# Kernel tuning notes

Measured on AMD Instinct MI355X. Metric: run time of the kernel, lower is better.

The kernel has to match this reference:

```python
import jax, jax.numpy as jnp
import numpy as np

B, G, T = 4096, 100, 24


def _greedy_dispatch(demand, caps, prices, slack_price):
    """Exact LP solution of: min prices@alloc + slack_price*slack
    s.t. 0<=alloc<=caps, sum(alloc)+slack = demand (per b,t).
    demand: [B,T] (nonneg), caps: [B,G,T], prices: [G], slack_price: scalar.
    Returns alloc [B,G,T], slack [B,T].
    """
    prices_all = jnp.concatenate([prices, slack_price[None]])        # [G+1]
    # slack capacity = demand itself (slack alone can absorb everything)
    caps_all = jnp.concatenate([caps, demand[:, None, :]], axis=1)    # [B,G+1,T]
    order = jnp.argsort(prices_all)                                   # merit order
    caps_s = caps_all[:, order, :]
    before = jnp.cumsum(caps_s, axis=1) - caps_s                      # capacity ahead in merit order
    alloc_s = jnp.clip(demand[:, None, :] - before, 0.0, caps_s)
    inv = jnp.argsort(order)
    alloc = alloc_s[:, inv, :]
    return alloc[:, :-1, :], alloc[:, -1, :]


def setup_inputs() -> dict:
    key = jax.random.key(0)
    k1, k2, k3, k4 = jax.random.split(key, 4)
    R_up = jax.random.uniform(k1, (B, G, T), dtype=jnp.float32)
    R_dn = jax.random.uniform(k2, (B, G, T), dtype=jnp.float32)
    omega_true = jax.random.normal(k3, (B, T), dtype=jnp.float32) * 5.0
    b_G = 10.0 + 40.0 * jax.random.uniform(k4, (G,), dtype=jnp.float32)  # marginal costs $/MWh
    return {
        "R_up": R_up,
        "R_dn": R_dn,
        "omega_true": omega_true,
        "b_G": b_G,
        "voll": jnp.float32(1000.0),
        "vosp": jnp.float32(500.0),
        "rt_up_ratio": jnp.float32(1.5),
        "rt_dn_ratio": jnp.float32(1.2),
    }


def reference(R_up, R_dn, omega_true, b_G, voll, vosp, rt_up_ratio, rt_dn_ratio):
    c_up = rt_up_ratio * b_G                                          # [G]
    c_dn = rt_dn_ratio * b_G                                          # [G]
    dem_up = jnp.maximum(omega_true, 0.0)                             # [B,T]
    dem_dn = jnp.maximum(-omega_true, 0.0)
    du, LS = _greedy_dispatch(dem_up, R_up, c_up, voll)
    dd, SP = _greedy_dispatch(dem_dn, R_dn, c_dn, vosp)
    rt_obj = (jnp.einsum('g,bgt->b', c_up, du)
              + jnp.einsum('g,bgt->b', c_dn, dd)
              + voll * LS.sum(axis=1) + vosp * SP.sum(axis=1))        # [B]
    return du, dd, LS, SP, rt_obj
```

## Files before the change

### kernel.cpp

```cpp
#include <hip/hip_runtime.h>

#define G_ 100
#define T_ 24
#define GP1 101
#define TILE (G_ * T_)
#define VPB (TILE / 4)
#define BPB 4
#define WPB (BPB * 2)
#define BLOCK (64 * WPB)

typedef float vfloat4 __attribute__((ext_vector_type(4)));

template<int N>
__device__ __forceinline__ void scan_chunk(int k0,
    const float* __restrict__ capp,
    float* __restrict__ gcol,
    int ord_lo, int ord_hi, float pr_lo, float pr_hi,
    float dem, float& before, float& objp)
{
    int gg[N]; float pr[N], cap[N];
#pragma unroll
    for (int j = 0; j < N; ++j) {
        const int idx = k0 + j;
        if (idx < 64) {
            gg[j] = __builtin_amdgcn_readlane(ord_lo, idx);
            pr[j] = __int_as_float(__builtin_amdgcn_readlane(__float_as_int(pr_lo), idx));
        } else {
            gg[j] = __builtin_amdgcn_readlane(ord_hi, idx - 64);
            pr[j] = __int_as_float(__builtin_amdgcn_readlane(__float_as_int(pr_hi), idx - 64));
        }
    }
#pragma unroll
    for (int j = 0; j < N; ++j) cap[j] = capp[gg[j] * T_];
#pragma unroll
    for (int j = 0; j < N; ++j) {
        float a = fminf(fmaxf(dem - before, 0.f), cap[j]);
        before += cap[j];
        objp = fmaf(pr[j], a, objp);
        gcol[gg[j] * T_] = a;
    }
}

__global__ __launch_bounds__(BLOCK, 8) void dispatch_kernel(
    const float* __restrict__ R_up, const float* __restrict__ R_dn,
    const float* __restrict__ omega,
    const float* __restrict__ b_G, const float* __restrict__ voll,
    const float* __restrict__ vosp, const float* __restrict__ ru,
    const float* __restrict__ rd,
    float* __restrict__ out, int B)
{
    __shared__ float s_praw[2][GP1];
    __shared__ int   s_ord [2][128];
    __shared__ float s_pr  [2][128];
    __shared__ float s_obj [WPB];

    const int tid = threadIdx.x;

    if (tid < GP1) {
        float mu, md;
        if (tid < G_) { float bg = b_G[tid]; mu = ru[0] * bg; md = rd[0] * bg; }
        else          { mu = voll[0];        md = vosp[0]; }
        s_praw[0][tid] = mu; s_praw[1][tid] = md;
    }
    __syncthreads();
    {
        const int pass = tid >> 8;
        const int i    = tid & 255;
        if (i < GP1) {
            const float m = s_praw[pass][i];
            int r = 0;
            for (int j = 0; j < GP1; ++j) {
                const float v = s_praw[pass][j];
                r += (v < m) || (v == m && j < i);
            }
            s_ord[pass][r] = i;  s_pr[pass][r] = m;
        }
    }
    __syncthreads();

    const int w    = tid >> 6;
    const int lane = tid & 63;
    const int b = __builtin_amdgcn_readfirstlane(blockIdx.x * BPB + (w >> 1));
    const int p = __builtin_amdgcn_readfirstlane(w & 1);
    const size_t bgt = (size_t)B * TILE;

    const int hi_ok = (lane < GP1 - 64);
    const int   ord_lo = s_ord[p][lane];
    const int   ord_hi = hi_ok ? s_ord[p][64 + lane] : 0;
    const float pr_lo  = s_pr [p][lane];
    const float pr_hi  = hi_ok ? s_pr [p][64 + lane] : 0.f;

    const int t = (lane < T_) ? lane : 0;

    float objp = 0.f;
    if (lane < T_) {
        const float om  = omega[(size_t)b * T_ + t];
        const float dem = p ? fmaxf(-om, 0.f) : fmaxf(om, 0.f);
        const float* __restrict__ capp = (p ? R_dn : R_up) + (size_t)b * TILE + t;
        float* __restrict__ gcol = out + (size_t)p * bgt + (size_t)b * TILE + t;

        float before = 0.f;
        scan_chunk<16>( 0, capp, gcol, ord_lo, ord_hi, pr_lo, pr_hi, dem, before, objp);
        scan_chunk<16>(16, capp, gcol, ord_lo, ord_hi, pr_lo, pr_hi, dem, before, objp);
        int K = 32;
        bool run = __any(before < dem);
        if (run) { scan_chunk<16>(32, capp, gcol, ord_lo, ord_hi, pr_lo, pr_hi, dem, before, objp);
                   K = 48; run = __any(before < dem); }
        if (run) { scan_chunk<16>(48, capp, gcol, ord_lo, ord_hi, pr_lo, pr_hi, dem, before, objp);
                   K = 64; run = __any(before < dem); }
        if (run) { scan_chunk< 8>(64, capp, gcol, ord_lo, ord_hi, pr_lo, pr_hi, dem, before, objp);
                   K = 72; run = __any(before < dem); }
        if (run) { scan_chunk< 8>(72, capp, gcol, ord_lo, ord_hi, pr_lo, pr_hi, dem, before, objp);
                   K = 80; run = __any(before < dem); }
        if (run) { scan_chunk< 8>(80, capp, gcol, ord_lo, ord_hi, pr_lo, pr_hi, dem, before, objp);
                   K = 88; run = __any(before < dem); }
        if (run) { scan_chunk< 8>(88, capp, gcol, ord_lo, ord_hi, pr_lo, pr_hi, dem, before, objp);
                   K = 96; run = __any(before < dem); }
        if (run) { scan_chunk< 4>(96, capp, gcol, ord_lo, ord_hi, pr_lo, pr_hi, dem, before, objp);
                   K = 100; }

        for (int r = K; r < G_; ++r) {
            const int g = (r < 64) ? __builtin_amdgcn_readlane(ord_lo, r)
                                   : __builtin_amdgcn_readlane(ord_hi, r - 64);
            gcol[g * T_] = 0.f;
        }

        const float slack_pr =
            __int_as_float(__builtin_amdgcn_readlane(__float_as_int(pr_hi), GP1 - 1 - 64));
        float slackv = fmaxf(dem - before, 0.f);
        objp = fmaf(slack_pr, slackv, objp);
        out[2 * bgt + (size_t)p * B * T_ + (size_t)b * T_ + t] = slackv;
    }

#pragma unroll
    for (int off = 32; off; off >>= 1) objp += __shfl_xor(objp, off, 64);
    if (lane == 0) s_obj[w] = objp;

    __syncthreads();
    if ((tid & 127) == 0)
        out[2 * bgt + 2 * (size_t)B * T_ + b] = s_obj[w] + s_obj[w + 1];
}

extern "C" void kernel_launch(void* const* d_in, const int* in_sizes, int n_in,
                              void* d_out, int out_size, void* d_ws, size_t ws_size,
                              hipStream_t stream)
{
    const float* R_up  = (const float*)d_in[0];
    const float* R_dn  = (const float*)d_in[1];
    const float* omega = (const float*)d_in[2];
    const float* b_G   = (const float*)d_in[3];
    const float* voll  = (const float*)d_in[4];
    const float* vosp  = (const float*)d_in[5];
    const float* ru    = (const float*)d_in[6];
    const float* rd    = (const float*)d_in[7];

    const int B = in_sizes[0] / TILE;
    float* out = (float*)d_out;

    dispatch_kernel<<<B / BPB, BLOCK, 0, stream>>>(
        R_up, R_dn, omega, b_G, voll, vosp, ru, rd, out, B);
}
```

Baseline: 163.4 us.

## Pack one (batch, direction, hour) column per thread instead of per wave

Threads are remapped so every lane handles one (b, direction, t) column: 8 batches × 2 directions × 24 hours gives 384 threads. Previously each 64-lane wave handled one (b, direction) and left 40 lanes idle. A single shared merit-order sort of b_G now replaces the two per-direction sorts, with prices rebuilt as ratio×b_G and slack priced separately. The per-batch objective is reduced through shared memory instead of a wave shuffle. Because each wave now mixes several batches, the early-exit __any checks are less likely to fire, and stores within a wave now span multiple tiles.

```diff
diff --git a/kernel.cpp b/kernel.cpp
--- a/kernel.cpp
+++ b/kernel.cpp
@@ -2,12 +2,9 @@
 
 #define G_ 100
 #define T_ 24
-#define GP1 101
 #define TILE (G_ * T_)
-#define VPB (TILE / 4)
-#define BPB 4
-#define WPB (BPB * 2)
-#define BLOCK (64 * WPB)
+#define BPB 8
+#define BLOCK (BPB * 2 * T_)
 
 typedef float vfloat4 __attribute__((ext_vector_type(4)));
 
@@ -15,7 +12,7 @@
 __device__ __forceinline__ void scan_chunk(int k0,
     const float* __restrict__ capp,
     float* __restrict__ gcol,
-    int ord_lo, int ord_hi, float pr_lo, float pr_hi,
+    int ord_lo, int ord_hi, float bg_lo, float bg_hi, float ratio,
     float dem, float& before, float& objp)
 {
     int gg[N]; float pr[N], cap[N];
@@ -24,10 +21,12 @@
         const int idx = k0 + j;
         if (idx < 64) {
             gg[j] = __builtin_amdgcn_readlane(ord_lo, idx);
-            pr[j] = __int_as_float(__builtin_amdgcn_readlane(__float_as_int(pr_lo), idx));
+            pr[j] = ratio * __int_as_float(
+                        __builtin_amdgcn_readlane(__float_as_int(bg_lo), idx));
         } else {
             gg[j] = __builtin_amdgcn_readlane(ord_hi, idx - 64);
-            pr[j] = __int_as_float(__builtin_amdgcn_readlane(__float_as_int(pr_hi), idx - 64));
+            pr[j] = ratio * __int_as_float(
+                        __builtin_amdgcn_readlane(__float_as_int(bg_hi), idx - 64));
         }
     }
 #pragma unroll
@@ -49,96 +48,83 @@
     const float* __restrict__ rd,
     float* __restrict__ out, int B)
 {
-    __shared__ float s_praw[2][GP1];
-    __shared__ int   s_ord [2][128];
-    __shared__ float s_pr  [2][128];
-    __shared__ float s_obj [WPB];
+    __shared__ float s_bgraw[G_];
+    __shared__ int   s_ord[128];
+    __shared__ float s_bgs[128];
+    __shared__ float s_oc[BLOCK];
 
     const int tid = threadIdx.x;
 
-    if (tid < GP1) {
-        float mu, md;
-        if (tid < G_) { float bg = b_G[tid]; mu = ru[0] * bg; md = rd[0] * bg; }
-        else          { mu = voll[0];        md = vosp[0]; }
-        s_praw[0][tid] = mu; s_praw[1][tid] = md;
-    }
+    if (tid < G_) s_bgraw[tid] = b_G[tid];
+    if (tid >= G_ && tid < 128) { s_ord[tid] = 0; s_bgs[tid] = 0.f; }
     __syncthreads();
-    {
-        const int pass = tid >> 8;
-        const int i    = tid & 255;
-        if (i < GP1) {
-            const float m = s_praw[pass][i];
-            int r = 0;
-            for (int j = 0; j < GP1; ++j) {
-                const float v = s_praw[pass][j];
-                r += (v < m) || (v == m && j < i);
-            }
-            s_ord[pass][r] = i;  s_pr[pass][r] = m;
+    if (tid < G_) {
+        const float m = s_bgraw[tid];
+        int r = 0;
+        for (int j = 0; j < G_; ++j) {
+            const float v = s_bgraw[j];
+            r += (v < m) || (v == m && j < tid);
         }
+        s_ord[r] = tid;  s_bgs[r] = m;
     }
     __syncthreads();
 
-    const int w    = tid >> 6;
     const int lane = tid & 63;
-    const int b = __builtin_amdgcn_readfirstlane(blockIdx.x * BPB + (w >> 1));
-    const int p = __builtin_amdgcn_readfirstlane(w & 1);
+    const int pi = tid / (BPB * T_);
+    const int rm = tid % (BPB * T_);
+    const int b  = blockIdx.x * BPB + rm / T_;
+    const int t  = rm % T_;
     const size_t bgt = (size_t)B * TILE;
 
-    const int hi_ok = (lane < GP1 - 64);
-    const int   ord_lo = s_ord[p][lane];
-    const int   ord_hi = hi_ok ? s_ord[p][64 + lane] : 0;
-    const float pr_lo  = s_pr [p][lane];
-    const float pr_hi  = hi_ok ? s_pr [p][64 + lane] : 0.f;
+    const int hi_ok = (lane < G_ - 64);
+    const int   ord_lo = s_ord[lane];
+    const int   ord_hi = hi_ok ? s_ord[64 + lane] : 0;
+    const float bg_lo  = s_bgs[lane];
+    const float bg_hi  = hi_ok ? s_bgs[64 + lane] : 0.f;
 
-    const int t = (lane < T_) ? lane : 0;
+    const float ratio    = pi ? rd[0]   : ru[0];
+    const float slack_pr = pi ? vosp[0] : voll[0];
 
-    float objp = 0.f;
-    if (lane < T_) {
-        const float om  = omega[(size_t)b * T_ + t];
-        const float dem = p ? fmaxf(-om, 0.f) : fmaxf(om, 0.f);
-        const float* __restrict__ capp = (p ? R_dn : R_up) + (size_t)b * TILE + t;
-        float* __restrict__ gcol = out + (size_t)p * bgt + (size_t)b * TILE + t;
+    const float om  = omega[(size_t)b * T_ + t];
+    const float dem = pi ? fmaxf(-om, 0.f) : fmaxf(om, 0.f);
+    const float* __restrict__ capp = (pi ? R_dn : R_up) + (size_t)b * TILE + t;
+    float* __restrict__ gcol = out + (size_t)pi * bgt + (size_t)b * TILE + t;
 
-        float before = 0.f;
-        scan_chunk<16>( 0, capp, gcol, ord_lo, ord_hi, pr_lo, pr_hi, dem, before, objp);
-        scan_chunk<16>(16, capp, gcol, ord_lo, ord_hi, pr_lo, pr_hi, dem, before, objp);
-        int K = 32;
-        bool run = __any(before < dem);
-        if (run) { scan_chunk<16>(32, capp, gcol, ord_lo, ord_hi, pr_lo, pr_hi, dem, before, objp);
-                   K = 48; run = __any(before < dem); }
-        if (run) { scan_chunk<16>(48, capp, gcol, ord_lo, ord_hi, pr_lo, pr_hi, dem, before, objp);
-                   K = 64; run = __any(before < dem); }
-        if (run) { scan_chunk< 8>(64, capp, gcol, ord_lo, ord_hi, pr_lo, pr_hi, dem, before, objp);
-                   K = 72; run = __any(before < dem); }
-        if (run) { scan_chunk< 8>(72, capp, gcol, ord_lo, ord_hi, pr_lo, pr_hi, dem, before, objp);
-                   K = 80; run = __any(before < dem); }
-        if (run) { scan_chunk< 8>(80, capp, gcol, ord_lo, ord_hi, pr_lo, pr_hi, dem, before, objp);
-                   K = 88; run = __any(before < dem); }
-        if (run) { scan_chunk< 8>(88, capp, gcol, ord_lo, ord_hi, pr_lo, pr_hi, dem, before, objp);
-                   K = 96; run = __any(before < dem); }
-        if (run) { scan_chunk< 4>(96, capp, gcol, ord_lo, ord_hi, pr_lo, pr_hi, dem, before, objp);
-                   K = 100; }
+    float before = 0.f, objp = 0.f;
+    scan_chunk<32>( 0, capp, gcol, ord_lo, ord_hi, bg_lo, bg_hi, ratio, dem, before, objp);
+    int K = 32;
+    bool run = __any(before < dem);
+    if (run) { scan_chunk<16>(32, capp, gcol, ord_lo, ord_hi, bg_lo, bg_hi, ratio, dem, before, objp);
+               K = 48; run = __any(before < dem); }
+    if (run) { scan_chunk<16>(48, capp, gcol, ord_lo, ord_hi, bg_lo, bg_hi, ratio, dem, before, objp);
+               K = 64; run = __any(before < dem); }
+    if (run) { scan_chunk<16>(64, capp, gcol, ord_lo, ord_hi, bg_lo, bg_hi, ratio, dem, before, objp);
+               K = 80; run = __any(before < dem); }
+    if (run) { scan_chunk<16>(80, capp, gcol, ord_lo, ord_hi, bg_lo, bg_hi, ratio, dem, before, objp);
+               K = 96; run = __any(before < dem); }
+    if (run) { scan_chunk< 4>(96, capp, gcol, ord_lo, ord_hi, bg_lo, bg_hi, ratio, dem, before, objp);
+               K = 100; }
 
-        for (int r = K; r < G_; ++r) {
-            const int g = (r < 64) ? __builtin_amdgcn_readlane(ord_lo, r)
-                                   : __builtin_amdgcn_readlane(ord_hi, r - 64);
-            gcol[g * T_] = 0.f;
-        }
-
-        const float slack_pr =
-            __int_as_float(__builtin_amdgcn_readlane(__float_as_int(pr_hi), GP1 - 1 - 64));
-        float slackv = fmaxf(dem - before, 0.f);
-        objp = fmaf(slack_pr, slackv, objp);
-        out[2 * bgt + (size_t)p * B * T_ + (size_t)b * T_ + t] = slackv;
+    for (int r = K; r < G_; ++r) {
+        const int g = (r < 64) ? __builtin_amdgcn_readlane(ord_lo, r)
+                               : __builtin_amdgcn_readlane(ord_hi, r - 64);
+        gcol[g * T_] = 0.f;
     }
 
+    const float slackv = fmaxf(dem - before, 0.f);
+    objp = fmaf(slack_pr, slackv, objp);
+    out[2 * bgt + (size_t)pi * B * T_ + (size_t)b * T_ + t] = slackv;
+
+    s_oc[tid] = objp;
+    __syncthreads();
+    if (tid < BPB * T_) s_oc[tid] += s_oc[tid + BPB * T_];
+    __syncthreads();
+    if (tid < BPB) {
+        float s = 0.f;
 #pragma unroll
-    for (int off = 32; off; off >>= 1) objp += __shfl_xor(objp, off, 64);
-    if (lane == 0) s_obj[w] = objp;
-
-    __syncthreads();
-    if ((tid & 127) == 0)
-        out[2 * bgt + 2 * (size_t)B * T_ + b] = s_obj[w] + s_obj[w + 1];
+        for (int j = 0; j < T_; ++j) s += s_oc[tid * T_ + j];
+        out[2 * bgt + 2 * (size_t)B * T_ + (size_t)blockIdx.x * BPB + tid] = s;
+    }
 }
 
 extern "C" void kernel_launch(void* const* d_in, const int* in_sizes, int n_in,
```

Result: no change. 164.2 us (+0.5%).
